# Optimization experiments

Measured on AMD Instinct MI355X. Metric: run time of the kernel, lower is better.

## Reference

```python
import jax, jax.numpy as jnp
import numpy as np

B, T, U = 8, 200, 100
E, P, H, V = 512, 640, 512, 1024


def setup_inputs() -> dict:
    key = jax.random.key(0)
    ks = jax.random.split(key, 8)
    def xavier(k, fan_in, fan_out, gain=0.1):
        bound = gain * np.sqrt(6.0 / (fan_in + fan_out))
        return jax.random.uniform(k, (fan_out, fan_in), jnp.float32, -bound, bound)
    return {
        "encoder_outputs": jax.random.normal(ks[0], (B, T, E), jnp.float32),
        "predictor_outputs": jax.random.normal(ks[1], (B, U, P), jnp.float32),
        "W_enc": xavier(ks[2], E, H),
        "b_enc": jnp.zeros((H,), jnp.float32),
        "W_pred": xavier(ks[3], P, H),
        "b_pred": jnp.zeros((H,), jnp.float32),
        "W_out": xavier(ks[4], H, V),
        "b_out": jnp.zeros((V,), jnp.float32),
    }


def reference(encoder_outputs, predictor_outputs, W_enc, b_enc, W_pred, b_pred, W_out, b_out):
    # project: (B,T,H) and (B,U,H)
    enc = jnp.einsum('bte,he->bth', encoder_outputs, W_enc) + b_enc
    pred = jnp.einsum('bup,hp->buh', predictor_outputs, W_pred) + b_pred
    # broadcast add -> (B,T,U,H), relu (dropout is identity at eval)
    joint = jax.nn.relu(enc[:, :, None, :] + pred[:, None, :, :])
    # output projection -> (B,T,U,V), scaled by 0.1
    out = jnp.einsum('btuh,vh->btuv', joint, W_out) + b_out
    return out * 0.1
```

## Files before the change

kernel.cpp:

```cpp
#include <hip/hip_runtime.h>
#include <hip/hip_bf16.h>
#include <cstdint>
#include <cstddef>

typedef __attribute__((ext_vector_type(8))) __bf16 bf16x8;
typedef __attribute__((ext_vector_type(4))) __bf16 bf16x4;
typedef __attribute__((ext_vector_type(4))) float  f32x4;

#define B_  8
#define T_  200
#define U_  100
#define E_  512
#define P_  640
#define H_  512
#define V_  1024

__device__ __forceinline__ void async_ld16(const void* g, void* lds) {
  __builtin_amdgcn_global_load_lds(
      (const __attribute__((address_space(1))) unsigned int*)g,
      (__attribute__((address_space(3))) unsigned int*)lds,
      16, 0, 0);
}

__global__ __launch_bounds__(256)
void cvt_all_kernel(const float* s0, __bf16* d0, const float* s1, __bf16* d1,
                    const float* s2, __bf16* d2, const float* s3, __bf16* d3,
                    const float* s4, __bf16* d4,
                    int e0, int e1, int e2, int e3) {
  int blk = blockIdx.x;
  const float* s; __bf16* d; int base;
  if      (blk < e0) { s = s0; d = d0; base = blk; }
  else if (blk < e1) { s = s1; d = d1; base = blk - e0; }
  else if (blk < e2) { s = s2; d = d2; base = blk - e1; }
  else if (blk < e3) { s = s3; d = d3; base = blk - e2; }
  else               { s = s4; d = d4; base = blk - e3; }
  int i = base * 1024 + threadIdx.x * 4;
  f32x4 v = *(const f32x4*)(s + i);
  bf16x4 o;
  o[0] = (__bf16)v[0]; o[1] = (__bf16)v[1]; o[2] = (__bf16)v[2]; o[3] = (__bf16)v[3];
  *(bf16x4*)(d + i) = o;
}

__global__ __launch_bounds__(256)
void build_joint_kernel(const float* __restrict__ enc, const float* __restrict__ pred,
                        __bf16* __restrict__ out) {
  int m    = blockIdx.x * 4 + (threadIdx.x >> 6);
  int lane = threadIdx.x & 63;
  int h0   = lane * 8;
  int bt = m / U_;
  int u  = m - bt * U_;
  int b  = bt / T_;
  const float* ep = enc  + (size_t)bt * H_ + h0;
  const float* pp = pred + ((size_t)b * U_ + u) * H_ + h0;
  f32x4 e0 = *(const f32x4*)ep, e1 = *(const f32x4*)(ep + 4);
  f32x4 p0 = *(const f32x4*)pp, p1 = *(const f32x4*)(pp + 4);
  bf16x8 q;
#pragma unroll
  for (int i = 0; i < 4; ++i) {
    q[i]     = (__bf16)fmaxf(e0[i] + p0[i], 0.f);
    q[i + 4] = (__bf16)fmaxf(e1[i] + p1[i], 0.f);
  }
  *(bf16x8*)(out + (size_t)m * H_ + h0) = q;
}

__global__ __launch_bounds__(256)
void gemm_bias_kernel(const __bf16* __restrict__ A, const __bf16* __restrict__ Bm,
                      const float* __restrict__ bias, float* __restrict__ C,
                      int M, int K, int ldc, float scale) {
  __shared__ __bf16 As[128 * 32];
  __shared__ __bf16 Bs[128 * 32];

  const int tid  = threadIdx.x;
  const int wave = tid >> 6, lane = tid & 63;
  const int l15  = lane & 15, quad = lane >> 4;
  const int wm   = wave & 1,  wn   = wave >> 1;
  const int m0 = blockIdx.y * 128, n0 = blockIdx.x * 128;

  f32x4 acc[4][4];
#pragma unroll
  for (int i = 0; i < 4; ++i)
#pragma unroll
    for (int j = 0; j < 4; ++j) acc[i][j] = (f32x4){0.f, 0.f, 0.f, 0.f};

  for (int kk = 0; kk < K; kk += 32) {
#pragma unroll
    for (int j = 0; j < 2; ++j) {
      int f   = (wave * 2 + j) * 1024 + lane * 16;
      int row = f >> 6;
      int kb  = (f & 63) >> 1;
      int ar  = m0 + row; if (ar >= M) ar = M - 1;
      async_ld16(A  + (size_t)ar * K + kk + kb,        (char*)As + (wave * 2 + j) * 1024);
      async_ld16(Bm + (size_t)(n0 + row) * K + kk + kb,(char*)Bs + (wave * 2 + j) * 1024);
    }
    __syncthreads();
    bf16x8 af[4], bfr[4];
#pragma unroll
    for (int mi = 0; mi < 4; ++mi)
      af[mi] = *(const bf16x8*)(As + (wm * 64 + mi * 16 + l15) * 32 + quad * 8);
#pragma unroll
    for (int ni = 0; ni < 4; ++ni)
      bfr[ni] = *(const bf16x8*)(Bs + (wn * 64 + ni * 16 + l15) * 32 + quad * 8);
#pragma unroll
    for (int mi = 0; mi < 4; ++mi)
#pragma unroll
      for (int ni = 0; ni < 4; ++ni)
        acc[mi][ni] = __builtin_amdgcn_mfma_f32_16x16x32_bf16(af[mi], bfr[ni], acc[mi][ni], 0, 0, 0);
    __syncthreads();
  }

#pragma unroll
  for (int ni = 0; ni < 4; ++ni) {
    int n = n0 + wn * 64 + ni * 16 + l15;
    float bo = bias[n];
#pragma unroll
    for (int mi = 0; mi < 4; ++mi) {
      int mb = m0 + wm * 64 + mi * 16 + quad * 4;
#pragma unroll
      for (int r = 0; r < 4; ++r) {
        int m = mb + r;
        if (m < M) C[(size_t)m * ldc + n] = (acc[mi][ni][r] + bo) * scale;
      }
    }
  }
}

__global__ __launch_bounds__(256)
void fused_joint_kernel(const float* __restrict__ enc, const float* __restrict__ pred,
                        const __bf16* __restrict__ Wout, const float* __restrict__ b_out,
                        float* __restrict__ out) {
  __shared__ __bf16 As[128 * 40];
  __shared__ __bf16 Bs[128 * 32];

  const int tid  = threadIdx.x;
  const int wave = tid >> 6, lane = tid & 63;
  const int l15  = lane & 15, quad = lane >> 4;
  const int wm   = wave & 1,  wn   = wave >> 1;
  const int n0 = blockIdx.x * 128;
  const int m0 = blockIdx.y * 128;

  const int r   = tid >> 1;
  const int kof = (tid & 1) << 4;
  const int m   = m0 + r;
  const int u   = m % U_;
  const int bt  = m / U_;
  const int b   = bt / T_;
  const float* encp  = enc  + (size_t)bt * H_ + kof;
  const float* predp = pred + ((size_t)b * U_ + u) * H_ + kof;
  __bf16* asp = As + r * 40 + kof;

  f32x4 acc[4][4];
#pragma unroll
  for (int i = 0; i < 4; ++i)
#pragma unroll
    for (int j = 0; j < 4; ++j) acc[i][j] = (f32x4){0.f, 0.f, 0.f, 0.f};

  for (int kk = 0; kk < H_; kk += 32) {
#pragma unroll
    for (int j = 0; j < 2; ++j) {
      int f   = (wave * 2 + j) * 1024 + lane * 16;
      int row = f >> 6;
      int kb  = (f & 63) >> 1;
      async_ld16(Wout + (size_t)(n0 + row) * H_ + kk + kb, (char*)Bs + (wave * 2 + j) * 1024);
    }
    f32x4 ef[4], pf[4];
#pragma unroll
    for (int i = 0; i < 4; ++i) {
      ef[i] = *(const f32x4*)(encp  + kk + i * 4);
      pf[i] = *(const f32x4*)(predp + kk + i * 4);
    }
    bf16x8 q0, q1;
#pragma unroll
    for (int i = 0; i < 8; ++i) {
      float v0 = fmaxf(ef[i >> 2][i & 3] + pf[i >> 2][i & 3], 0.f);
      float v1 = fmaxf(ef[(i + 8) >> 2][(i + 8) & 3] + pf[(i + 8) >> 2][(i + 8) & 3], 0.f);
      q0[i] = (__bf16)v0;
      q1[i] = (__bf16)v1;
    }
    *(bf16x8*)asp       = q0;
    *((bf16x8*)asp + 1) = q1;
    __syncthreads();

    bf16x8 af[4], bfr[4];
#pragma unroll
    for (int mi = 0; mi < 4; ++mi)
      af[mi] = *(const bf16x8*)(As + (wm * 64 + mi * 16 + l15) * 40 + quad * 8);
#pragma unroll
    for (int ni = 0; ni < 4; ++ni)
      bfr[ni] = *(const bf16x8*)(Bs + (wn * 64 + ni * 16 + l15) * 32 + quad * 8);
#pragma unroll
    for (int mi = 0; mi < 4; ++mi)
#pragma unroll
      for (int ni = 0; ni < 4; ++ni)
        acc[mi][ni] = __builtin_amdgcn_mfma_f32_16x16x32_bf16(af[mi], bfr[ni], acc[mi][ni], 0, 0, 0);
    __syncthreads();
  }

#pragma unroll
  for (int ni = 0; ni < 4; ++ni) {
    int n = n0 + wn * 64 + ni * 16 + l15;
    float bo = b_out[n];
#pragma unroll
    for (int mi = 0; mi < 4; ++mi) {
      size_t mb = (size_t)m0 + wm * 64 + mi * 16 + quad * 4;
      float* op = out + mb * V_ + n;
#pragma unroll
      for (int rr = 0; rr < 4; ++rr)
        op[(size_t)rr * V_] = (acc[mi][ni][rr] + bo) * 0.1f;
    }
  }
}

extern "C" void kernel_launch(void* const* d_in, const int* in_sizes, int n_in,
                              void* d_out, int out_size, void* d_ws, size_t ws_size,
                              hipStream_t stream) {
  const float* encoder   = (const float*)d_in[0];
  const float* predictor = (const float*)d_in[1];
  const float* W_enc     = (const float*)d_in[2];
  const float* b_enc     = (const float*)d_in[3];
  const float* W_pred    = (const float*)d_in[4];
  const float* b_pred    = (const float*)d_in[5];
  const float* W_out     = (const float*)d_in[6];
  const float* b_out     = (const float*)d_in[7];
  float* out = (float*)d_out;

  char* ws = (char*)d_ws;
  size_t off = 0;
  auto alloc = [&](size_t bytes) { char* p = ws + off; off += (bytes + 255) & ~(size_t)255; return p; };

  float*  enc_f    = (float*)alloc((size_t)1600 * 512 * 4);
  float*  pred_f   = (float*)alloc((size_t)800 * 512 * 4);
  __bf16* enc_bf   = (__bf16*)alloc((size_t)1600 * 512 * 2);
  __bf16* Wenc_bf  = (__bf16*)alloc((size_t)512 * 512 * 2);
  __bf16* pred_bf  = (__bf16*)alloc((size_t)800 * 640 * 2);
  __bf16* Wpred_bf = (__bf16*)alloc((size_t)512 * 640 * 2);
  __bf16* Wout_bf  = (__bf16*)alloc((size_t)1024 * 512 * 2);
  __bf16* joint_bf = (__bf16*)alloc((size_t)160000 * 512 * 2);
  bool big_ws = (off <= ws_size);

  cvt_all_kernel<<<2388, 256, 0, stream>>>(
      encoder, enc_bf, W_enc, Wenc_bf, predictor, pred_bf, W_pred, Wpred_bf,
      W_out, Wout_bf, 800, 1056, 1556, 1876);

  gemm_bias_kernel<<<dim3(4, 13), 256, 0, stream>>>(enc_bf, Wenc_bf, b_enc, enc_f, 1600, 512, 512, 1.0f);
  gemm_bias_kernel<<<dim3(4, 7), 256, 0, stream>>>(pred_bf, Wpred_bf, b_pred, pred_f, 800, 640, 512, 1.0f);

  if (big_ws) {
    build_joint_kernel<<<160000 / 4, 256, 0, stream>>>(enc_f, pred_f, joint_bf);
    gemm_bias_kernel<<<dim3(8, 1250), 256, 0, stream>>>(joint_bf, Wout_bf, b_out, out,
                                                        160000, 512, 1024, 0.1f);
  } else {
    fused_joint_kernel<<<dim3(8, 1250), 256, 0, stream>>>(enc_f, pred_f, Wout_bf, b_out, out);
  }
}
```

Baseline: 1.115 ms.

## Always fuse joint build into output GEMM with 128x256 tiles, merge projection GEMMs

Drops the materialized bf16 joint tensor path and always builds the relu(enc+pred) tile on the fly inside the output GEMM. That GEMM now uses 512-thread blocks covering 256 output columns, with operands swapped so each lane holds four consecutive columns and writes vectorized f32x4 stores. The two projection GEMMs are merged into one launch using blockIdx.z. This removes the large joint tensor write and re-read plus one launch, at the cost of more register and LDS use per block.

```diff
diff --git a/kernel.cpp b/kernel.cpp
--- a/kernel.cpp
+++ b/kernel.cpp
@@ -42,31 +42,18 @@
 }
 
 __global__ __launch_bounds__(256)
-void build_joint_kernel(const float* __restrict__ enc, const float* __restrict__ pred,
-                        __bf16* __restrict__ out) {
-  int m    = blockIdx.x * 4 + (threadIdx.x >> 6);
-  int lane = threadIdx.x & 63;
-  int h0   = lane * 8;
-  int bt = m / U_;
-  int u  = m - bt * U_;
-  int b  = bt / T_;
-  const float* ep = enc  + (size_t)bt * H_ + h0;
-  const float* pp = pred + ((size_t)b * U_ + u) * H_ + h0;
-  f32x4 e0 = *(const f32x4*)ep, e1 = *(const f32x4*)(ep + 4);
-  f32x4 p0 = *(const f32x4*)pp, p1 = *(const f32x4*)(pp + 4);
-  bf16x8 q;
-#pragma unroll
-  for (int i = 0; i < 4; ++i) {
-    q[i]     = (__bf16)fmaxf(e0[i] + p0[i], 0.f);
-    q[i + 4] = (__bf16)fmaxf(e1[i] + p1[i], 0.f);
-  }
-  *(bf16x8*)(out + (size_t)m * H_ + h0) = q;
-}
-
-__global__ __launch_bounds__(256)
-void gemm_bias_kernel(const __bf16* __restrict__ A, const __bf16* __restrict__ Bm,
-                      const float* __restrict__ bias, float* __restrict__ C,
-                      int M, int K, int ldc, float scale) {
+void gemm_dual_kernel(const __bf16* __restrict__ A0, const __bf16* __restrict__ B0,
+                      const float* __restrict__ bias0, float* __restrict__ C0, int M0, int K0,
+                      const __bf16* __restrict__ A1, const __bf16* __restrict__ B1,
+                      const float* __restrict__ bias1, float* __restrict__ C1, int M1, int K1,
+                      int ytiles1) {
+  const __bf16* A;  const __bf16* Bm;  const float* bias;  float* C;  int M, K;
+  if (blockIdx.z == 0) { A = A0; Bm = B0; bias = bias0; C = C0; M = M0; K = K0; }
+  else {
+    if ((int)blockIdx.y >= ytiles1) return;
+    A = A1; Bm = B1; bias = bias1; C = C1; M = M1; K = K1;
+  }
+
   __shared__ __bf16 As[128 * 32];
   __shared__ __bf16 Bs[128 * 32];
 
@@ -118,32 +105,32 @@
 #pragma unroll
       for (int r = 0; r < 4; ++r) {
         int m = mb + r;
-        if (m < M) C[(size_t)m * ldc + n] = (acc[mi][ni][r] + bo) * scale;
+        if (m < M) C[(size_t)m * 512 + n] = acc[mi][ni][r] + bo;
       }
     }
   }
 }
 
-__global__ __launch_bounds__(256)
-void fused_joint_kernel(const float* __restrict__ enc, const float* __restrict__ pred,
-                        const __bf16* __restrict__ Wout, const float* __restrict__ b_out,
-                        float* __restrict__ out) {
+__global__ __launch_bounds__(512, 4)
+void fused_joint256_kernel(const float* __restrict__ enc, const float* __restrict__ pred,
+                           const __bf16* __restrict__ Wout, const float* __restrict__ b_out,
+                           float* __restrict__ out) {
   __shared__ __bf16 As[128 * 40];
-  __shared__ __bf16 Bs[128 * 32];
+  __shared__ __bf16 Bs[256 * 32];
 
   const int tid  = threadIdx.x;
   const int wave = tid >> 6, lane = tid & 63;
   const int l15  = lane & 15, quad = lane >> 4;
   const int wm   = wave & 1,  wn   = wave >> 1;
-  const int n0 = blockIdx.x * 128;
+  const int n0 = blockIdx.x * 256;
   const int m0 = blockIdx.y * 128;
 
-  const int r   = tid >> 1;
-  const int kof = (tid & 1) << 4;
-  const int m   = m0 + r;
-  const int u   = m % U_;
-  const int bt  = m / U_;
-  const int b   = bt / T_;
+  const int r    = tid >> 2;
+  const int kof  = (tid & 3) << 3;
+  const int m    = m0 + r;
+  const int bt   = m / U_;
+  const int u    = m - bt * U_;
+  const int b    = bt / T_;
   const float* encp  = enc  + (size_t)bt * H_ + kof;
   const float* predp = pred + ((size_t)b * U_ + u) * H_ + kof;
   __bf16* asp = As + r * 40 + kof;
@@ -157,27 +144,22 @@
   for (int kk = 0; kk < H_; kk += 32) {
 #pragma unroll
     for (int j = 0; j < 2; ++j) {
-      int f   = (wave * 2 + j) * 1024 + lane * 16;
+      int f   = j * 8192 + tid * 16;
       int row = f >> 6;
       int kb  = (f & 63) >> 1;
-      async_ld16(Wout + (size_t)(n0 + row) * H_ + kk + kb, (char*)Bs + (wave * 2 + j) * 1024);
-    }
-    f32x4 ef[4], pf[4];
+      async_ld16(Wout + (size_t)(n0 + row) * H_ + kk + kb, (char*)Bs + f);
+    }
+    f32x4 e0 = *(const f32x4*)(encp  + kk);
+    f32x4 e1 = *(const f32x4*)(encp  + kk + 4);
+    f32x4 p0 = *(const f32x4*)(predp + kk);
+    f32x4 p1 = *(const f32x4*)(predp + kk + 4);
+    bf16x8 q;
 #pragma unroll
     for (int i = 0; i < 4; ++i) {
-      ef[i] = *(const f32x4*)(encp  + kk + i * 4);
-      pf[i] = *(const f32x4*)(predp + kk + i * 4);
-    }
-    bf16x8 q0, q1;
-#pragma unroll
-    for (int i = 0; i < 8; ++i) {
-      float v0 = fmaxf(ef[i >> 2][i & 3] + pf[i >> 2][i & 3], 0.f);
-      float v1 = fmaxf(ef[(i + 8) >> 2][(i + 8) & 3] + pf[(i + 8) >> 2][(i + 8) & 3], 0.f);
-      q0[i] = (__bf16)v0;
-      q1[i] = (__bf16)v1;
-    }
-    *(bf16x8*)asp       = q0;
-    *((bf16x8*)asp + 1) = q1;
+      q[i]     = (__bf16)fmaxf(e0[i] + p0[i], 0.f);
+      q[i + 4] = (__bf16)fmaxf(e1[i] + p1[i], 0.f);
+    }
+    *(bf16x8*)asp = q;
     __syncthreads();
 
     bf16x8 af[4], bfr[4];
@@ -188,24 +170,24 @@
     for (int ni = 0; ni < 4; ++ni)
       bfr[ni] = *(const bf16x8*)(Bs + (wn * 64 + ni * 16 + l15) * 32 + quad * 8);
 #pragma unroll
-    for (int mi = 0; mi < 4; ++mi)
-#pragma unroll
-      for (int ni = 0; ni < 4; ++ni)
-        acc[mi][ni] = __builtin_amdgcn_mfma_f32_16x16x32_bf16(af[mi], bfr[ni], acc[mi][ni], 0, 0, 0);
+    for (int ni = 0; ni < 4; ++ni)
+#pragma unroll
+      for (int mi = 0; mi < 4; ++mi)
+        acc[ni][mi] = __builtin_amdgcn_mfma_f32_16x16x32_bf16(bfr[ni], af[mi], acc[ni][mi], 0, 0, 0);
     __syncthreads();
   }
 
 #pragma unroll
   for (int ni = 0; ni < 4; ++ni) {
-    int n = n0 + wn * 64 + ni * 16 + l15;
-    float bo = b_out[n];
+    int nb = n0 + wn * 64 + ni * 16 + quad * 4;
+    f32x4 bo = *(const f32x4*)(b_out + nb);
 #pragma unroll
     for (int mi = 0; mi < 4; ++mi) {
-      size_t mb = (size_t)m0 + wm * 64 + mi * 16 + quad * 4;
-      float* op = out + mb * V_ + n;
-#pragma unroll
-      for (int rr = 0; rr < 4; ++rr)
-        op[(size_t)rr * V_] = (acc[mi][ni][rr] + bo) * 0.1f;
+      int mm = m0 + wm * 64 + mi * 16 + l15;
+      f32x4 v;
+#pragma unroll
+      for (int rr = 0; rr < 4; ++rr) v[rr] = (acc[ni][mi][rr] + bo[rr]) * 0.1f;
+      *(f32x4*)(out + (size_t)mm * V_ + nb) = v;
     }
   }
 }
@@ -234,21 +216,15 @@
   __bf16* pred_bf  = (__bf16*)alloc((size_t)800 * 640 * 2);
   __bf16* Wpred_bf = (__bf16*)alloc((size_t)512 * 640 * 2);
   __bf16* Wout_bf  = (__bf16*)alloc((size_t)1024 * 512 * 2);
-  __bf16* joint_bf = (__bf16*)alloc((size_t)160000 * 512 * 2);
-  bool big_ws = (off <= ws_size);
+  (void)ws_size;
 
   cvt_all_kernel<<<2388, 256, 0, stream>>>(
       encoder, enc_bf, W_enc, Wenc_bf, predictor, pred_bf, W_pred, Wpred_bf,
       W_out, Wout_bf, 800, 1056, 1556, 1876);
 
-  gemm_bias_kernel<<<dim3(4, 13), 256, 0, stream>>>(enc_bf, Wenc_bf, b_enc, enc_f, 1600, 512, 512, 1.0f);
-  gemm_bias_kernel<<<dim3(4, 7), 256, 0, stream>>>(pred_bf, Wpred_bf, b_pred, pred_f, 800, 640, 512, 1.0f);
-
-  if (big_ws) {
-    build_joint_kernel<<<160000 / 4, 256, 0, stream>>>(enc_f, pred_f, joint_bf);
-    gemm_bias_kernel<<<dim3(8, 1250), 256, 0, stream>>>(joint_bf, Wout_bf, b_out, out,
-                                                        160000, 512, 1024, 0.1f);
-  } else {
-    fused_joint_kernel<<<dim3(8, 1250), 256, 0, stream>>>(enc_f, pred_f, Wout_bf, b_out, out);
-  }
-}
+  gemm_dual_kernel<<<dim3(4, 13, 2), 256, 0, stream>>>(
+      enc_bf,  Wenc_bf,  b_enc,  enc_f,  1600, 512,
+      pred_bf, Wpred_bf, b_pred, pred_f,  800, 640, 7);
+
+  fused_joint256_kernel<<<dim3(4, 1250), 512, 0, stream>>>(enc_f, pred_f, Wout_bf, b_out, out);
+}
```

New measurement: 895.7 us. 1.24x faster.
